# Performance work log

Measured on AMD Instinct MI355X. Metric: run time of the kernel, lower is better.

Reference implementation:

```python
import jax, jax.numpy as jnp
import numpy as np

N = 50000        # nodes
E = 800000       # edges (before self-loops)
IN = 128         # in_channels
HID = 32         # hidden_channels
HEADS = 8        # num_heads
G = 64           # num graphs in batch
NEG_SLOPE = 0.2  # PyG GATConv default


def setup_inputs() -> dict:
    key = jax.random.key(0)
    ks = jax.random.split(key, 12)
    x = jax.random.normal(ks[0], (N, IN), jnp.float32)
    edge_index = jax.random.randint(ks[1], (2, E), 0, N, jnp.int32)
    edge_attr = jax.random.normal(ks[2], (E, 4), jnp.float32)
    batch = jnp.sort(jax.random.randint(ks[3], (N,), 0, G, jnp.int32))
    s = 0.05
    # GATConv 1: in -> HEADS*HID
    W1 = jax.random.normal(ks[4], (IN, HEADS * HID), jnp.float32) * s
    a_src1 = jax.random.normal(ks[5], (HEADS, HID), jnp.float32) * s
    a_dst1 = jax.random.normal(ks[6], (HEADS, HID), jnp.float32) * s
    b1 = jnp.zeros((HEADS * HID,), jnp.float32)
    # GATConv 2: HEADS*HID -> HID (heads=1)
    W2 = jax.random.normal(ks[7], (HEADS * HID, HID), jnp.float32) * s
    a_src2 = jax.random.normal(ks[8], (1, HID), jnp.float32) * s
    a_dst2 = jax.random.normal(ks[9], (1, HID), jnp.float32) * s
    b2 = jnp.zeros((HID,), jnp.float32)
    return {"x": x, "edge_index": edge_index, "edge_attr": edge_attr, "batch": batch,
            "W1": W1, "a_src1": a_src1, "a_dst1": a_dst1, "b1": b1,
            "W2": W2, "a_src2": a_src2, "a_dst2": a_dst2, "b2": b2}


def gat_conv(x, src, dst, W, a_src, a_dst, b):
    # x: [N, F_in]; W: [F_in, H*C]; a_src/a_dst: [H, C]
    H, C = a_src.shape
    h = (x @ W).reshape(N, H, C)                      # [N, H, C]
    al_s = jnp.einsum('nhc,hc->nh', h, a_src)         # [N, H]
    al_d = jnp.einsum('nhc,hc->nh', h, a_dst)
    e = jax.nn.leaky_relu(al_s[src] + al_d[dst], NEG_SLOPE)  # [Etot, H]
    # segment softmax over incoming edges of each dst node
    m = jax.ops.segment_max(e, dst, num_segments=N)
    p = jnp.exp(e - m[dst])
    z = jax.ops.segment_sum(p, dst, num_segments=N)
    alpha = p / z[dst]                                # [Etot, H]
    out = jax.ops.segment_sum(alpha[:, :, None] * h[src], dst, num_segments=N)
    return out.reshape(N, H * C) + b


def reference(x, edge_index, edge_attr, batch, W1, a_src1, a_dst1, b1, W2, a_src2, a_dst2, b2):
    # edge_attr is ignored: GATConv was built without edge_dim (PyG lin_edge=None).
    loops = jnp.arange(N, dtype=edge_index.dtype)     # PyG add_self_loops=True
    src = jnp.concatenate([edge_index[0], loops])
    dst = jnp.concatenate([edge_index[1], loops])
    h = jax.nn.relu(gat_conv(x, src, dst, W1, a_src1, a_dst1, b1))
    # dropout p=0.2 is identity in eval mode
    h = gat_conv(h, src, dst, W2, a_src2, a_dst2, b2)  # [N, HID]
    # global_mean_pool over graph ids
    sums = jax.ops.segment_sum(h, batch, num_segments=G)
    cnts = jax.ops.segment_sum(jnp.ones((N, 1), h.dtype), batch, num_segments=G)
    return sums / jnp.maximum(cnts, 1.0)              # [G, HID]
```

## Files before the change

### kernel.cpp

```cpp
#include <hip/hip_runtime.h>
#include <hip/hip_bf16.h>

#define NNODES 50000
#define NEDGES 800000
#define FIN 128
#define HID 32
#define HEADS 8
#define NG 64
#define NEG_SLOPE 0.2f
#define MAXDEG 64

using bf16x8 = __attribute__((ext_vector_type(8))) short;
using f32x4  = __attribute__((ext_vector_type(4))) float;

static __device__ __forceinline__ float leaky(float x) {
    return x > 0.f ? x : NEG_SLOPE * x;
}
static __device__ __forceinline__ unsigned short f2bf(float f) {
    unsigned int x = __float_as_uint(f);
    return (unsigned short)((x + 0x7FFFu + ((x >> 16) & 1u)) >> 16);
}
static __device__ __forceinline__ unsigned int pack2bf(float lo, float hi) {
    return (unsigned int)f2bf(lo) | ((unsigned int)f2bf(hi) << 16);
}
static __device__ __forceinline__ float bfl(unsigned int u) {
    return __uint_as_float(u << 16);
}
static __device__ __forceinline__ float bfh(unsigned int u) {
    return __uint_as_float(u & 0xFFFF0000u);
}
static __device__ __forceinline__ float bfs(unsigned short u) {
    return __uint_as_float((unsigned int)u << 16);
}

#define ZERO_BLOCKS 196
__global__ void zero_swz_kernel(int* __restrict__ cnt,
                                const float* __restrict__ W1, const float* __restrict__ W2,
                                unsigned short* __restrict__ w1s,
                                unsigned short* __restrict__ w2s) {
    if (blockIdx.x < ZERO_BLOCKS) {
        int i = blockIdx.x * 256 + threadIdx.x;
        if (i < NNODES) cnt[i] = 0;
        return;
    }
    int idx = (blockIdx.x - ZERO_BLOCKS) * 256 + threadIdx.x;
    if (idx < 32768) {
        int j    = idx & 7;
        int lane = (idx >> 3) & 63;
        int ks   = (idx >> 9) & 3;
        int ct   = idx >> 11;
        int k = ks * 32 + (lane >> 4) * 8 + j;
        int n = ct * 16 + (lane & 15);
        w1s[idx] = f2bf(W1[k * 256 + n]);
    } else if (idx < 32768 + 8192) {
        int id2  = idx - 32768;
        int j    = id2 & 7;
        int lane = (id2 >> 3) & 63;
        int ks   = (id2 >> 9) & 7;
        int ct   = id2 >> 12;
        int k = ks * 32 + (lane >> 4) * 8 + j;
        int n = ct * 16 + (lane & 15);
        w2s[id2] = f2bf(W2[k * 32 + n]);
    }
}

#define GEMM1_BLOCKS 782
__global__ __launch_bounds__(256) void gemm1_scatter_kernel(const float* __restrict__ x,
                                                            const unsigned short* __restrict__ w1s,
                                                            const float* __restrict__ a_src,
                                                            const float* __restrict__ a_dst,
                                                            unsigned short* __restrict__ h1b,
                                                            float* __restrict__ al_s,
                                                            float* __restrict__ al_d,
                                                            const int* __restrict__ ei,
                                                            int* __restrict__ cnt,
                                                            unsigned short* __restrict__ csr) {
    __shared__ unsigned short lds[4][16 * 64];
    if (blockIdx.x >= GEMM1_BLOCKS) {
        int e = (blockIdx.x - GEMM1_BLOCKS) * 256 + threadIdx.x;
        if (e < NEDGES) {
            int s = ei[e];
            int d = ei[NEDGES + e];
            int pos = atomicAdd(&cnt[d], 1);
            csr[(d << 6) + pos] = (unsigned short)s;
        }
        return;
    }
    int t = threadIdx.x;
    int w = t >> 6;
    int l = t & 63;
    int lane16 = l & 15, quad = l >> 4;

    bf16x8 bf[4][4];
    const bf16x8* wp = (const bf16x8*)w1s;
#pragma unroll
    for (int ct = 0; ct < 4; ++ct)
#pragma unroll
        for (int ks = 0; ks < 4; ++ks)
            bf[ct][ks] = wp[((w * 4 + ct) * 4 + ks) * 64 + l];

    float as_c[4], ad_c[4];
#pragma unroll
    for (int ct = 0; ct < 4; ++ct) {
        int col = w * 64 + ct * 16 + lane16;
        as_c[ct] = a_src[col];
        ad_c[ct] = a_dst[col];
    }

    int rbase = blockIdx.x * 64;
    for (int rg = 0; rg < 4; ++rg) {
        int row0 = rbase + rg * 16;
        int r = row0 + lane16;
        int r_eff = r < NNODES ? r : NNODES - 1;
        bf16x8 af[4];
#pragma unroll
        for (int ks = 0; ks < 4; ++ks) {
            const float* ap = x + (size_t)r_eff * FIN + ks * 32 + quad * 8;
            float4 a0 = *(const float4*)ap;
            float4 a1 = *(const float4*)(ap + 4);
            bf16x8 v;
            v[0] = (short)f2bf(a0.x); v[1] = (short)f2bf(a0.y);
            v[2] = (short)f2bf(a0.z); v[3] = (short)f2bf(a0.w);
            v[4] = (short)f2bf(a1.x); v[5] = (short)f2bf(a1.y);
            v[6] = (short)f2bf(a1.z); v[7] = (short)f2bf(a1.w);
            af[ks] = v;
        }
        f32x4 acc[4];
#pragma unroll
        for (int ct = 0; ct < 4; ++ct) acc[ct] = (f32x4){0.f, 0.f, 0.f, 0.f};
#pragma unroll
        for (int ks = 0; ks < 4; ++ks)
#pragma unroll
            for (int ct = 0; ct < 4; ++ct)
                acc[ct] = __builtin_amdgcn_mfma_f32_16x16x32_bf16(af[ks], bf[ct][ks], acc[ct], 0, 0, 0);

#pragma unroll
        for (int reg = 0; reg < 4; ++reg) {
            float ps0 = acc[0][reg] * as_c[0] + acc[1][reg] * as_c[1];
            float ps1 = acc[2][reg] * as_c[2] + acc[3][reg] * as_c[3];
            float pd0 = acc[0][reg] * ad_c[0] + acc[1][reg] * ad_c[1];
            float pd1 = acc[2][reg] * ad_c[2] + acc[3][reg] * ad_c[3];
#pragma unroll
            for (int m = 1; m < 16; m <<= 1) {
                ps0 += __shfl_xor(ps0, m); ps1 += __shfl_xor(ps1, m);
                pd0 += __shfl_xor(pd0, m); pd1 += __shfl_xor(pd1, m);
            }
            int gr = row0 + quad * 4 + reg;
            if (lane16 == 0 && gr < NNODES) {
                al_s[gr * HEADS + 2 * w]     = ps0;
                al_s[gr * HEADS + 2 * w + 1] = ps1;
                al_d[gr * HEADS + 2 * w]     = pd0;
                al_d[gr * HEADS + 2 * w + 1] = pd1;
            }
        }

        unsigned short* lw = lds[w];
#pragma unroll
        for (int ct = 0; ct < 4; ++ct)
#pragma unroll
            for (int reg = 0; reg < 4; ++reg)
                lw[(quad * 4 + reg) * 64 + ct * 16 + lane16] = f2bf(acc[ct][reg]);
        int row_l = l >> 2;
        int ch = l & 3;
        int gr = row0 + row_l;
        if (gr < NNODES) {
            const uint4* srcp = (const uint4*)(lw + row_l * 64 + ch * 16);
            uint4 d0 = srcp[0];
            uint4 d1 = srcp[1];
            uint4* dst = (uint4*)(h1b + (size_t)gr * 256 + w * 64 + ch * 16);
            dst[0] = d0;
            dst[1] = d1;
        }
    }
}

__global__ __launch_bounds__(256) void gather1_kernel(const unsigned short* __restrict__ h1b,
                                                      const float* __restrict__ al_s,
                                                      const float* __restrict__ al_d,
                                                      const int* __restrict__ cnt,
                                                      const unsigned short* __restrict__ csr,
                                                      const float* __restrict__ b1,
                                                      unsigned short* __restrict__ out1b) {
    int t = threadIdx.x;
    int l = t & 63;
    int q = l & 31;
    int base = l & 32;
    int n = blockIdx.x * 8 + (t >> 5);
    int e_st = q >> 3;
    int h_st = q & 7;
    int h_f  = q >> 2;
    float ad_st = al_d[n * HEADS + h_st];

    float p = __expf(leaky(al_s[n * HEADS + h_f] + al_d[n * HEADS + h_f]));
    float z = p;
    float acc[8];
    {
        uint4 v = *(const uint4*)(h1b + (size_t)n * 256 + q * 8);
        acc[0] = p * bfl(v.x); acc[1] = p * bfh(v.x);
        acc[2] = p * bfl(v.y); acc[3] = p * bfh(v.y);
        acc[4] = p * bfl(v.z); acc[5] = p * bfh(v.z);
        acc[6] = p * bfl(v.w); acc[7] = p * bfh(v.w);
    }

    int beg = n << 6;
    int end = beg + cnt[n];
    for (int i = beg; i < end; i += 4) {
        int rem = end - i;
        int src4 = n;
        float pe4 = 0.f;
        if (e_st < rem) {
            src4 = csr[i + e_st];
            pe4 = __expf(leaky(al_s[src4 * HEADS + h_st] + ad_st));
        }
#pragma unroll
        for (int j = 0; j < 4; ++j) {
            int   sj  = __shfl(src4, base + j * 8);
            float pej = __shfl(pe4, base + j * 8 + h_f);
            uint4 v = *(const uint4*)(h1b + (size_t)sj * 256 + q * 8);
            z += pej;
            acc[0] += pej * bfl(v.x); acc[1] += pej * bfh(v.x);
            acc[2] += pej * bfl(v.y); acc[3] += pej * bfh(v.y);
            acc[4] += pej * bfl(v.z); acc[5] += pej * bfh(v.z);
            acc[6] += pej * bfl(v.w); acc[7] += pej * bfh(v.w);
        }
    }
    float inv = 1.0f / z;
    float4 b0 = *(const float4*)(b1 + q * 8);
    float4 b2 = *(const float4*)(b1 + q * 8 + 4);
    float o[8];
    o[0] = acc[0] * inv + b0.x; o[1] = acc[1] * inv + b0.y;
    o[2] = acc[2] * inv + b0.z; o[3] = acc[3] * inv + b0.w;
    o[4] = acc[4] * inv + b2.x; o[5] = acc[5] * inv + b2.y;
    o[6] = acc[6] * inv + b2.z; o[7] = acc[7] * inv + b2.w;
#pragma unroll
    for (int k = 0; k < 8; ++k) o[k] = o[k] > 0.f ? o[k] : 0.f;
    uint4 pk;
    pk.x = pack2bf(o[0], o[1]); pk.y = pack2bf(o[2], o[3]);
    pk.z = pack2bf(o[4], o[5]); pk.w = pack2bf(o[6], o[7]);
    *(uint4*)(out1b + (size_t)n * 256 + q * 8) = pk;
}

__global__ __launch_bounds__(256) void gemm2_mfma_kernel(const unsigned short* __restrict__ out1b,
                                                         const unsigned short* __restrict__ w2s,
                                                         const float* __restrict__ a_src,
                                                         const float* __restrict__ a_dst,
                                                         unsigned short* __restrict__ h2b,
                                                         float* __restrict__ al_s,
                                                         float* __restrict__ al_d) {
    int t = threadIdx.x;
    int w = t >> 6;
    int l = t & 63;
    int lane16 = l & 15, quad = l >> 4;

    bf16x8 bf[2][8];
    const bf16x8* wp = (const bf16x8*)w2s;
#pragma unroll
    for (int ct = 0; ct < 2; ++ct)
#pragma unroll
        for (int ks = 0; ks < 8; ++ks)
            bf[ct][ks] = wp[((ct * 8 + ks)) * 64 + l];

    float as_c[2], ad_c[2];
#pragma unroll
    for (int ct = 0; ct < 2; ++ct) {
        as_c[ct] = a_src[ct * 16 + lane16];
        ad_c[ct] = a_dst[ct * 16 + lane16];
    }

    int row0 = blockIdx.x * 64 + w * 16;
    int r = row0 + lane16;
    int r_eff = r < NNODES ? r : NNODES - 1;
    f32x4 acc[2];
    acc[0] = (f32x4){0.f, 0.f, 0.f, 0.f};
    acc[1] = (f32x4){0.f, 0.f, 0.f, 0.f};
#pragma unroll
    for (int ks = 0; ks < 8; ++ks) {
        bf16x8 af = *(const bf16x8*)(out1b + (size_t)r_eff * 256 + ks * 32 + quad * 8);
        acc[0] = __builtin_amdgcn_mfma_f32_16x16x32_bf16(af, bf[0][ks], acc[0], 0, 0, 0);
        acc[1] = __builtin_amdgcn_mfma_f32_16x16x32_bf16(af, bf[1][ks], acc[1], 0, 0, 0);
    }
#pragma unroll
    for (int reg = 0; reg < 4; ++reg) {
        int gr = row0 + quad * 4 + reg;
        if (gr < NNODES) {
            h2b[(size_t)gr * 32 + lane16]      = f2bf(acc[0][reg]);
            h2b[(size_t)gr * 32 + 16 + lane16] = f2bf(acc[1][reg]);
        }
        float ps = acc[0][reg] * as_c[0] + acc[1][reg] * as_c[1];
        float pd = acc[0][reg] * ad_c[0] + acc[1][reg] * ad_c[1];
#pragma unroll
        for (int m = 1; m < 16; m <<= 1) {
            ps += __shfl_xor(ps, m);
            pd += __shfl_xor(pd, m);
        }
        if (lane16 == 0 && gr < NNODES) {
            al_s[gr] = ps;
            al_d[gr] = pd;
        }
    }
}

__global__ __launch_bounds__(256) void gather2_kernel(const unsigned short* __restrict__ h2b,
                                                      const float* __restrict__ al_s,
                                                      const float* __restrict__ al_d,
                                                      const int* __restrict__ cnt,
                                                      const unsigned short* __restrict__ csr,
                                                      const float* __restrict__ b2,
                                                      float* __restrict__ out2) {
    int t = threadIdx.x;
    int l = t & 63;
    int c = l & 31;
    int base = l & 32;
    int n = blockIdx.x * 8 + (t >> 5);
    float ad = al_d[n];
    float p = __expf(leaky(al_s[n] + ad));
    float z = p;
    float acc = p * bfs(h2b[(size_t)n * HID + c]);
    int beg = n << 6;
    int end = beg + cnt[n];
    for (int i = beg; i < end; i += 32) {
        int rem = end - i;
        int src = n;
        float pe = 0.f;
        if (c < rem) {
            src = csr[i + c];
            pe = __expf(leaky(al_s[src] + ad));
        }
        int m = rem < 32 ? rem : 32;
        for (int j0 = 0; j0 < m; j0 += 8) {
#pragma unroll
            for (int jj = 0; jj < 8; ++jj) {
                int   sj  = __shfl(src, base + j0 + jj);
                float pej = __shfl(pe, base + j0 + jj);
                z += pej;
                acc += pej * bfs(h2b[(size_t)sj * HID + c]);
            }
        }
    }
    out2[n * HID + c] = acc / z + b2[c];
}

__global__ __launch_bounds__(256) void pool_kernel(const float* __restrict__ out2,
                                                   const int* __restrict__ batch,
                                                   float* __restrict__ out) {
    __shared__ float red[256];
    int g = blockIdx.x;
    int t = threadIdx.x;
    int c = t & 31;
    int sub = t >> 5;
    int beg, end;
    {
        int lo = 0, hi = NNODES;
        while (lo < hi) { int mid = (lo + hi) >> 1; if (batch[mid] < g) lo = mid + 1; else hi = mid; }
        beg = lo;
        lo = beg; hi = NNODES;
        while (lo < hi) { int mid = (lo + hi) >> 1; if (batch[mid] < g + 1) lo = mid + 1; else hi = mid; }
        end = lo;
    }
    float s = 0.f;
    for (int n = beg + sub; n < end; n += 8) s += out2[n * HID + c];
    red[t] = s;
    __syncthreads();
    if (t < 32) {
        float tot = 0.f;
#pragma unroll
        for (int k = 0; k < 8; ++k) tot += red[c + 32 * k];
        int cnt2 = end - beg;
        out[g * HID + c] = tot / (float)(cnt2 > 0 ? cnt2 : 1);
    }
}

extern "C" void kernel_launch(void* const* d_in, const int* in_sizes, int n_in,
                              void* d_out, int out_size, void* d_ws, size_t ws_size,
                              hipStream_t stream) {
    const float* x      = (const float*)d_in[0];
    const int*   ei     = (const int*)d_in[1];
    const int*   batch  = (const int*)d_in[3];
    const float* W1     = (const float*)d_in[4];
    const float* a_src1 = (const float*)d_in[5];
    const float* a_dst1 = (const float*)d_in[6];
    const float* b1     = (const float*)d_in[7];
    const float* W2     = (const float*)d_in[8];
    const float* a_src2 = (const float*)d_in[9];
    const float* a_dst2 = (const float*)d_in[10];
    const float* b2     = (const float*)d_in[11];
    float* out = (float*)d_out;

    char* ws = (char*)d_ws;
    size_t off = 0;
    auto alloc = [&](size_t bytes) {
        size_t o = off;
        off = (off + bytes + 255) & ~(size_t)255;
        return o;
    };
    unsigned short* h1b   = (unsigned short*)(ws + alloc((size_t)NNODES * 256 * 2));
    unsigned short* out1b = (unsigned short*)(ws + alloc((size_t)NNODES * 256 * 2));
    unsigned short* h2b   = (unsigned short*)(ws + alloc((size_t)NNODES * HID * 2));
    unsigned short* w1s   = (unsigned short*)(ws + alloc((size_t)16 * 4 * 64 * 8 * 2));
    unsigned short* w2s   = (unsigned short*)(ws + alloc((size_t)2 * 8 * 64 * 8 * 2));
    float* out2   = (float*)(ws + alloc((size_t)NNODES * HID * 4));
    float* al_s1  = (float*)(ws + alloc((size_t)NNODES * HEADS * 4));
    float* al_d1  = (float*)(ws + alloc((size_t)NNODES * HEADS * 4));
    float* al_s2  = (float*)(ws + alloc((size_t)NNODES * 4));
    float* al_d2  = (float*)(ws + alloc((size_t)NNODES * 4));
    int*   cnt    = (int*)(ws + alloc((size_t)NNODES * 4));
    unsigned short* csr = (unsigned short*)(ws + alloc((size_t)NNODES * MAXDEG * 2));
    (void)ws_size;

    zero_swz_kernel<<<ZERO_BLOCKS + 160, 256, 0, stream>>>(cnt, W1, W2, w1s, w2s);
    gemm1_scatter_kernel<<<GEMM1_BLOCKS + 3125, 256, 0, stream>>>(x, w1s, a_src1, a_dst1,
                                                                  h1b, al_s1, al_d1,
                                                                  ei, cnt, csr);
    gather1_kernel<<<NNODES / 8, 256, 0, stream>>>(h1b, al_s1, al_d1, cnt, csr, b1, out1b);

    gemm2_mfma_kernel<<<(NNODES + 63) / 64, 256, 0, stream>>>(out1b, w2s, a_src2, a_dst2,
                                                              h2b, al_s2, al_d2);
    gather2_kernel<<<NNODES / 8, 256, 0, stream>>>(h2b, al_s2, al_d2, cnt, csr, b2, out2);
    pool_kernel<<<NG, 256, 0, stream>>>(out2, batch, out);
}
```

Before: 297.2 us.

## Split edge scatter into XCD-partitioned kernel separate from GEMM1

Moves the CSR edge scatter out of the fused GEMM1 launch into its own kernel. In the new kernel each block filters edges by destination range keyed to blockIdx&7, which assumes round-robin block-to-XCD placement so the atomics and CSR writes for a node range stay in one XCD's L2. Edges are read four at a time with int4 loads. In exchange, every edge's destination is read eight times, and the scatter no longer overlaps with GEMM1, adding one kernel launch.

```diff
diff --git a/kernel.cpp b/kernel.cpp
--- a/kernel.cpp
+++ b/kernel.cpp
@@ -64,28 +64,37 @@
     }
 }
 
-#define GEMM1_BLOCKS 782
-__global__ __launch_bounds__(256) void gemm1_scatter_kernel(const float* __restrict__ x,
-                                                            const unsigned short* __restrict__ w1s,
-                                                            const float* __restrict__ a_src,
-                                                            const float* __restrict__ a_dst,
-                                                            unsigned short* __restrict__ h1b,
-                                                            float* __restrict__ al_s,
-                                                            float* __restrict__ al_d,
-                                                            const int* __restrict__ ei,
-                                                            int* __restrict__ cnt,
-                                                            unsigned short* __restrict__ csr) {
+#define SCAT_GROUPS 782
+__global__ void scatter_kernel(const int* __restrict__ ei, int* __restrict__ cnt,
+                               unsigned short* __restrict__ csr) {
+    int xcd = blockIdx.x & 7;
+    int slice = blockIdx.x >> 3;
+    int e4 = slice * 256 + threadIdx.x;
+    int dlo = xcd * 6250;
+    int dhi = dlo + 6250;
+    if (e4 < NEDGES / 4) {
+        int4 d = *(const int4*)(ei + NEDGES + e4 * 4);
+        int4 s;
+        bool a0 = d.x >= dlo && d.x < dhi;
+        bool a1 = d.y >= dlo && d.y < dhi;
+        bool a2 = d.z >= dlo && d.z < dhi;
+        bool a3 = d.w >= dlo && d.w < dhi;
+        if (a0 | a1 | a2 | a3) s = *(const int4*)(ei + e4 * 4);
+        if (a0) { int p = atomicAdd(&cnt[d.x], 1); csr[(d.x << 6) + p] = (unsigned short)s.x; }
+        if (a1) { int p = atomicAdd(&cnt[d.y], 1); csr[(d.y << 6) + p] = (unsigned short)s.y; }
+        if (a2) { int p = atomicAdd(&cnt[d.z], 1); csr[(d.z << 6) + p] = (unsigned short)s.z; }
+        if (a3) { int p = atomicAdd(&cnt[d.w], 1); csr[(d.w << 6) + p] = (unsigned short)s.w; }
+    }
+}
+
+__global__ __launch_bounds__(256) void gemm1_mfma_kernel(const float* __restrict__ x,
+                                                         const unsigned short* __restrict__ w1s,
+                                                         const float* __restrict__ a_src,
+                                                         const float* __restrict__ a_dst,
+                                                         unsigned short* __restrict__ h1b,
+                                                         float* __restrict__ al_s,
+                                                         float* __restrict__ al_d) {
     __shared__ unsigned short lds[4][16 * 64];
-    if (blockIdx.x >= GEMM1_BLOCKS) {
-        int e = (blockIdx.x - GEMM1_BLOCKS) * 256 + threadIdx.x;
-        if (e < NEDGES) {
-            int s = ei[e];
-            int d = ei[NEDGES + e];
-            int pos = atomicAdd(&cnt[d], 1);
-            csr[(d << 6) + pos] = (unsigned short)s;
-        }
-        return;
-    }
     int t = threadIdx.x;
     int w = t >> 6;
     int l = t & 63;
@@ -408,9 +417,10 @@
     (void)ws_size;
 
     zero_swz_kernel<<<ZERO_BLOCKS + 160, 256, 0, stream>>>(cnt, W1, W2, w1s, w2s);
-    gemm1_scatter_kernel<<<GEMM1_BLOCKS + 3125, 256, 0, stream>>>(x, w1s, a_src1, a_dst1,
-                                                                  h1b, al_s1, al_d1,
-                                                                  ei, cnt, csr);
+    scatter_kernel<<<SCAT_GROUPS * 8, 256, 0, stream>>>(ei, cnt, csr);
+
+    gemm1_mfma_kernel<<<(NNODES + 63) / 64, 256, 0, stream>>>(x, w1s, a_src1, a_dst1,
+                                                              h1b, al_s1, al_d1);
     gather1_kernel<<<NNODES / 8, 256, 0, stream>>>(h1b, al_s1, al_d1, cnt, csr, b1, out1b);
 
     gemm2_mfma_kernel<<<(NNODES + 63) / 64, 256, 0, stream>>>(out1b, w2s, a_src2, a_dst2,
```

After: 287.7 us. 3.2% less time.
